# Kernel optimization log

Hardware: AMD Instinct MI355X
Metric: run time of the kernel (lower is better)

The kernel has to match this reference:

```python
import jax, jax.numpy as jnp
import numpy as np

N_NODES = 100000
N_EDGES = 1600000
IN_FEATS = 128
HID = 128      # 2 * n_hidden
OUT = 64       # n_hidden


def setup_inputs() -> dict:
    key = jax.random.key(0)
    ks = jax.random.split(key, 10)
    features = jax.random.normal(ks[0], (N_NODES, IN_FEATS), dtype=jnp.float32)
    src = jax.random.randint(ks[1], (N_EDGES,), 0, N_NODES)
    dst = jax.random.randint(ks[2], (N_EDGES,), 0, N_NODES)
    s0 = 1.0 / np.sqrt(IN_FEATS)
    s1 = 1.0 / np.sqrt(HID)
    W_self0 = jax.random.uniform(ks[3], (IN_FEATS, HID), minval=-s0, maxval=s0, dtype=jnp.float32)
    W_neigh0 = jax.random.uniform(ks[4], (IN_FEATS, HID), minval=-s0, maxval=s0, dtype=jnp.float32)
    b0 = jnp.zeros((HID,), dtype=jnp.float32)
    W_self1 = jax.random.uniform(ks[5], (HID, OUT), minval=-s1, maxval=s1, dtype=jnp.float32)
    W_neigh1 = jax.random.uniform(ks[6], (HID, OUT), minval=-s1, maxval=s1, dtype=jnp.float32)
    b1 = jnp.zeros((OUT,), dtype=jnp.float32)
    return {"features": features, "src": src, "dst": dst,
            "W_self0": W_self0, "W_neigh0": W_neigh0, "b0": b0,
            "W_self1": W_self1, "W_neigh1": W_neigh1, "b1": b1}


def _mean_agg(x, src, dst, n_nodes):
    # gather neighbor feats along edges, sum per destination, divide by in-degree
    summed = jax.ops.segment_sum(x[src], dst, num_segments=n_nodes)  # [N, d]
    deg = jax.ops.segment_sum(jnp.ones((src.shape[0],), x.dtype), dst, num_segments=n_nodes)
    deg = jnp.maximum(deg, 1.0)[:, None]
    return summed / deg


def _sage_layer(x, src, dst, W_self, W_neigh, b, act):
    agg = _mean_agg(x, src, dst, x.shape[0])
    out = x @ W_self + agg @ W_neigh + b
    return jax.nn.relu(out) if act else out


def reference(features, src, dst, W_self0, W_neigh0, b0, W_self1, W_neigh1, b1):
    h = _sage_layer(features, src, dst, W_self0, W_neigh0, b0, act=True)
    h = _sage_layer(h, src, dst, W_self1, W_neigh1, b1, act=False)
    return h
```

## Files before the change

kernel.cpp:

```cpp
#include <hip/hip_runtime.h>

#define N_NODES 100000
#define N_EDGES 1600000
#define CAP 56
#define OVF_CAP 8192
#define GBLK 782
#define BINS 391
#define BINCAP 4608
#define ABLK 1563

typedef unsigned int uint;
typedef unsigned short ushort;
typedef __attribute__((ext_vector_type(8))) short short8;
typedef __attribute__((ext_vector_type(4))) float f32x4;

__device__ __forceinline__ ushort f2bf(float f) {
  uint x = __float_as_uint(f);
  x += 0x7fffu + ((x >> 16) & 1u);
  return (ushort)(x >> 16);
}
__device__ __forceinline__ float bflo(uint u) {
  return __uint_as_float(u << 16);
}
__device__ __forceinline__ float bfhi(uint u) {
  return __uint_as_float(u & 0xffff0000u);
}
__device__ __forceinline__ f32x4 uplo(uint4 u) {
  return (f32x4){bflo(u.x), bfhi(u.x), bflo(u.y), bfhi(u.y)};
}
__device__ __forceinline__ f32x4 uphi(uint4 u) {
  return (f32x4){bflo(u.z), bfhi(u.z), bflo(u.w), bfhi(u.w)};
}

__global__ __launch_bounds__(256) void k_pb(
    const int* __restrict__ src, const int* __restrict__ dst,
    const float* __restrict__ feat, const float* __restrict__ Ws0,
    const float* __restrict__ Wn0, const float* __restrict__ Ws1,
    const float* __restrict__ Wn1, uint* __restrict__ gcursor,
    uint* __restrict__ binbuf, int* __restrict__ ovf_cnt,
    int* __restrict__ ovf, uint* __restrict__ fbfu, ushort* __restrict__ wp0,
    ushort* __restrict__ wp1) {
  __shared__ uint hist[BINS];
  __shared__ uint base[BINS];
  int b = blockIdx.x;
  int tid = threadIdx.x;
  if (b < GBLK) {
    for (int i = tid; i < BINS; i += 256) hist[i] = 0;
    __syncthreads();
    int e0 = b * 2048;
    uint val[8], bn[8], rk[8];
    int vld[8];
#pragma unroll
    for (int it = 0; it < 8; ++it) {
      int e = e0 + it * 256 + tid;
      vld[it] = (e < N_EDGES);
      if (vld[it]) {
        uint s = (uint)src[e];
        uint d = (uint)dst[e];
        bn[it] = d >> 8;
        rk[it] = atomicAdd(&hist[bn[it]], 1u);
        val[it] = s | ((d & 255u) << 17);
      }
    }
    __syncthreads();
    for (int i = tid; i < BINS; i += 256)
      base[i] = hist[i] ? atomicAdd(&gcursor[i], hist[i]) : 0u;
    __syncthreads();
#pragma unroll
    for (int it = 0; it < 8; ++it) {
      if (!vld[it]) continue;
      uint p = base[bn[it]] + rk[it];
      if (p < BINCAP) {
        binbuf[(size_t)bn[it] * BINCAP + p] = val[it];
      } else {
        int o = atomicAdd(ovf_cnt, 1);
        if (o < OVF_CAP) {
          ovf[2 * o] = (int)(val[it] & 0x1FFFFu);
          ovf[2 * o + 1] = (int)(bn[it] * 256 + (val[it] >> 17));
        }
      }
    }
    return;
  }
  if (b < GBLK + 25000) {
    int i = (b - GBLK) * 256 + tid;
    float2 v = reinterpret_cast<const float2*>(feat)[i];
    fbfu[i] = (uint)f2bf(v.x) | ((uint)f2bf(v.y) << 16);
    return;
  }
  int idx = (b - GBLK - 25000) * 256 + tid;
  if (idx < 32768) {
    int k = idx >> 7, n = idx & 127;
    float v = (k < 128) ? Ws0[k * 128 + n] : Wn0[(k - 128) * 128 + n];
    int s = k >> 5, q = (k >> 3) & 3, j = k & 7;
    int t = n >> 4, c = n & 15;
    wp0[(((s * 8 + t) * 64) + (q * 16 + c)) * 8 + j] = f2bf(v);
  } else {
    int i2 = idx - 32768;
    int k = i2 >> 7, n = i2 & 127;
    float v = (n < 64) ? Wn1[k * 64 + n] : Ws1[k * 64 + (n - 64)];
    int s = k >> 5, q = (k >> 3) & 3, j = k & 7;
    int t = n >> 4, c = n & 15;
    wp1[(((s * 8 + t) * 64) + (q * 16 + c)) * 8 + j] = f2bf(v);
  }
}

__global__ __launch_bounds__(256) void k_agg0(
    const uint4* __restrict__ fbf4, const uint* __restrict__ binbuf,
    const uint* __restrict__ gcursor, int* __restrict__ ovf_cnt,
    int* __restrict__ ovf, uint4* __restrict__ agg4) {
  __shared__ __attribute__((aligned(16))) int lbkt[64 * CAP];
  __shared__ uint lcnt[64];
  int bb = blockIdx.x;
  int tid = threadIdx.x;
  if (tid < 64) lcnt[tid] = 0;
  __syncthreads();
  int bin = bb >> 2, q2 = bb & 3;
  int ne = min((int)gcursor[bin], BINCAP);
  for (int i = tid; i < ne; i += 256) {
    uint v = binbuf[(size_t)bin * BINCAP + i];
    uint dl = v >> 17;
    if ((int)(dl >> 6) == q2) {
      int ldl = (int)(dl & 63u);
      uint pos = atomicAdd(&lcnt[ldl], 1u);
      if (pos < CAP) {
        lbkt[ldl * CAP + pos] = (int)(v & 0x1FFFFu);
      } else {
        int o = atomicAdd(ovf_cnt, 1);
        if (o < OVF_CAP) {
          ovf[2 * o] = (int)(v & 0x1FFFFu);
          ovf[2 * o + 1] = (bin * 256 + (int)dl) | (1 << 30);
        }
      }
    }
  }
  __syncthreads();
  int g = tid >> 4, li = tid & 15;
  const int4* lb4 = reinterpret_cast<const int4*>(lbkt);
  int oc = min(*ovf_cnt, OVF_CAP);
#pragma unroll
  for (int p = 0; p < 4; ++p) {
    int nl = p * 16 + g;
    int n = bb * 64 + nl;
    int c = (int)lcnt[nl];
    int kb = min(c, CAP);
    f32x4 accA = (f32x4){0.f, 0.f, 0.f, 0.f};
    f32x4 accB = (f32x4){0.f, 0.f, 0.f, 0.f};
    for (int j = 0; j < kb; j += 8) {
      int4 ia = lb4[nl * 14 + (j >> 2)];
      int4 ib = lb4[nl * 14 + (j >> 2) + 1];
      int s0 = ia.x;
      int s1 = (j + 1 < kb) ? ia.y : 0;
      int s2 = (j + 2 < kb) ? ia.z : 0;
      int s3 = (j + 3 < kb) ? ia.w : 0;
      int s4 = (j + 4 < kb) ? ib.x : 0;
      int s5 = (j + 5 < kb) ? ib.y : 0;
      int s6 = (j + 6 < kb) ? ib.z : 0;
      int s7 = (j + 7 < kb) ? ib.w : 0;
      uint4 u0 = fbf4[(size_t)s0 * 16 + li];
      uint4 u1 = fbf4[(size_t)s1 * 16 + li];
      uint4 u2 = fbf4[(size_t)s2 * 16 + li];
      uint4 u3 = fbf4[(size_t)s3 * 16 + li];
      uint4 u4 = fbf4[(size_t)s4 * 16 + li];
      uint4 u5 = fbf4[(size_t)s5 * 16 + li];
      uint4 u6 = fbf4[(size_t)s6 * 16 + li];
      uint4 u7 = fbf4[(size_t)s7 * 16 + li];
      float m1 = (j + 1 < kb) ? 1.f : 0.f;
      float m2 = (j + 2 < kb) ? 1.f : 0.f;
      float m3 = (j + 3 < kb) ? 1.f : 0.f;
      float m4 = (j + 4 < kb) ? 1.f : 0.f;
      float m5 = (j + 5 < kb) ? 1.f : 0.f;
      float m6 = (j + 6 < kb) ? 1.f : 0.f;
      float m7 = (j + 7 < kb) ? 1.f : 0.f;
      accA += uplo(u0);      accB += uphi(u0);
      accA += uplo(u1) * m1; accB += uphi(u1) * m1;
      accA += uplo(u2) * m2; accB += uphi(u2) * m2;
      accA += uplo(u3) * m3; accB += uphi(u3) * m3;
      accA += uplo(u4) * m4; accB += uphi(u4) * m4;
      accA += uplo(u5) * m5; accB += uphi(u5) * m5;
      accA += uplo(u6) * m6; accB += uphi(u6) * m6;
      accA += uplo(u7) * m7; accB += uphi(u7) * m7;
    }
    for (int i = 0; i < oc; ++i) {
      int df = ovf[2 * i + 1];
      if ((df & 0x1FFFF) == n) {
        uint4 u = fbf4[(size_t)ovf[2 * i] * 16 + li];
        accA += uplo(u);
        accB += uphi(u);
        c += ((df >> 30) & 1) ^ 1;
      }
    }
    float inv = 1.f / (float)max(c, 1);
    accA *= inv;
    accB *= inv;
    if (n < N_NODES) {
      uint4 o;
      o.x = (uint)f2bf(accA.x) | ((uint)f2bf(accA.y) << 16);
      o.y = (uint)f2bf(accA.z) | ((uint)f2bf(accA.w) << 16);
      o.z = (uint)f2bf(accB.x) | ((uint)f2bf(accB.y) << 16);
      o.w = (uint)f2bf(accB.z) | ((uint)f2bf(accB.w) << 16);
      agg4[(size_t)n * 16 + li] = o;
    }
  }
}

__global__ __launch_bounds__(256) void k_gemm0(
    const ushort* __restrict__ fbf, const ushort* aggb,
    const uint4* __restrict__ wp0g, const float* __restrict__ b0,
    ushort* h) {
  __shared__ uint4 wlds[4096];
  int tid = threadIdx.x;
#pragma unroll
  for (int i = 0; i < 16; ++i) wlds[i * 256 + tid] = wp0g[i * 256 + tid];
  __syncthreads();
  const short8* wl8 = reinterpret_cast<const short8*>(wlds);

  int lane = tid & 63, w = tid >> 6;
  int quad = lane >> 4, lm = lane & 15;
  int mw = blockIdx.x * 128 + (w >> 1) * 64;
  int tgb = (w & 1) * 4;

  f32x4 acc[4][4];
#pragma unroll
  for (int rt = 0; rt < 4; ++rt)
#pragma unroll
    for (int ct = 0; ct < 4; ++ct) acc[rt][ct] = (f32x4){0.f, 0.f, 0.f, 0.f};
  short8 az = {0, 0, 0, 0, 0, 0, 0, 0};

#pragma unroll
  for (int s = 0; s < 8; ++s) {
    const ushort* bsrc = (s < 4) ? fbf : aggb;
    int koff = (s & 3) * 32 + quad * 8;
    short8 a[4];
#pragma unroll
    for (int rt = 0; rt < 4; ++rt) {
      int row = mw + rt * 16 + lm;
      a[rt] = (row < N_NODES)
                  ? *reinterpret_cast<const short8*>(bsrc + (size_t)row * 128 + koff)
                  : az;
    }
#pragma unroll
    for (int ct = 0; ct < 4; ++ct) {
      short8 b = wl8[(s * 8 + tgb + ct) * 64 + lane];
#pragma unroll
      for (int rt = 0; rt < 4; ++rt)
        acc[rt][ct] =
            __builtin_amdgcn_mfma_f32_16x16x32_bf16(a[rt], b, acc[rt][ct], 0, 0, 0);
    }
  }

  __syncthreads();
  float bv[4];
#pragma unroll
  for (int ct = 0; ct < 4; ++ct) bv[ct] = b0[(tgb + ct) * 16 + lm];
#pragma unroll
  for (int rt = 0; rt < 4; ++rt)
#pragma unroll
    for (int ct = 0; ct < 4; ++ct)
#pragma unroll
      for (int i = 0; i < 4; ++i) {
        int row = mw + rt * 16 + quad * 4 + i;
        if (row < N_NODES) {
          int col = (tgb + ct) * 16 + lm;
          h[(size_t)row * 128 + col] = f2bf(fmaxf(acc[rt][ct][i] + bv[ct], 0.f));
        }
      }
}

__global__ __launch_bounds__(256) void k_gemm1(
    const ushort* __restrict__ h, const uint4* __restrict__ wp1g,
    const float* __restrict__ b1, ushort* __restrict__ hw,
    float* __restrict__ out) {
  __shared__ uint4 wlds[2048];
  int tid = threadIdx.x;
#pragma unroll
  for (int i = 0; i < 8; ++i) wlds[i * 256 + tid] = wp1g[i * 256 + tid];
  __syncthreads();
  const short8* wl8 = reinterpret_cast<const short8*>(wlds);

  int lane = tid & 63, w = tid >> 6;
  int quad = lane >> 4, lm = lane & 15;
  int mw = blockIdx.x * 128 + (w >> 1) * 64;
  int tgb = (w & 1) * 4;

  f32x4 acc[4][4];
#pragma unroll
  for (int rt = 0; rt < 4; ++rt)
#pragma unroll
    for (int ct = 0; ct < 4; ++ct) acc[rt][ct] = (f32x4){0.f, 0.f, 0.f, 0.f};
  short8 az = {0, 0, 0, 0, 0, 0, 0, 0};

#pragma unroll
  for (int s = 0; s < 4; ++s) {
    int koff = s * 32 + quad * 8;
    short8 a[4];
#pragma unroll
    for (int rt = 0; rt < 4; ++rt) {
      int row = mw + rt * 16 + lm;
      a[rt] = (row < N_NODES)
                  ? *reinterpret_cast<const short8*>(h + (size_t)row * 128 + koff)
                  : az;
    }
#pragma unroll
    for (int ct = 0; ct < 4; ++ct) {
      short8 b = wl8[(s * 8 + tgb + ct) * 64 + lane];
#pragma unroll
      for (int rt = 0; rt < 4; ++rt)
        acc[rt][ct] =
            __builtin_amdgcn_mfma_f32_16x16x32_bf16(a[rt], b, acc[rt][ct], 0, 0, 0);
    }
  }

  if ((w & 1) == 0) {
#pragma unroll
    for (int rt = 0; rt < 4; ++rt)
#pragma unroll
      for (int ct = 0; ct < 4; ++ct)
#pragma unroll
        for (int i = 0; i < 4; ++i) {
          int row = mw + rt * 16 + quad * 4 + i;
          if (row < N_NODES)
            hw[(size_t)row * 64 + ct * 16 + lm] = f2bf(acc[rt][ct][i]);
        }
  } else {
    float bv[4];
#pragma unroll
    for (int ct = 0; ct < 4; ++ct) bv[ct] = b1[ct * 16 + lm];
#pragma unroll
    for (int rt = 0; rt < 4; ++rt)
#pragma unroll
      for (int ct = 0; ct < 4; ++ct)
#pragma unroll
        for (int i = 0; i < 4; ++i) {
          int row = mw + rt * 16 + quad * 4 + i;
          if (row < N_NODES)
            out[(size_t)row * 64 + ct * 16 + lm] = acc[rt][ct][i] + bv[ct];
        }
  }
}

__global__ __launch_bounds__(256) void k_agg1(
    const uint4* __restrict__ hw4, const uint* __restrict__ binbuf,
    const uint* __restrict__ gcursor, int* __restrict__ ovf_cnt,
    int* __restrict__ ovf, float* __restrict__ out) {
  __shared__ __attribute__((aligned(16))) int lbkt[64 * CAP];
  __shared__ uint lcnt[64];
  int bb = blockIdx.x;
  int tid = threadIdx.x;
  if (tid < 64) lcnt[tid] = 0;
  __syncthreads();
  int bin = bb >> 2, q2 = bb & 3;
  int ne = min((int)gcursor[bin], BINCAP);
  for (int i = tid; i < ne; i += 256) {
    uint v = binbuf[(size_t)bin * BINCAP + i];
    uint dl = v >> 17;
    if ((int)(dl >> 6) == q2) {
      int ldl = (int)(dl & 63u);
      uint pos = atomicAdd(&lcnt[ldl], 1u);
      if (pos < CAP) lbkt[ldl * CAP + pos] = (int)(v & 0x1FFFFu);
    }
  }
  __syncthreads();
  int g = tid >> 3, li = tid & 7;
  const int4* lb4 = reinterpret_cast<const int4*>(lbkt);
  int oc = min(*ovf_cnt, OVF_CAP);
#pragma unroll
  for (int p = 0; p < 2; ++p) {
    int nl = p * 32 + g;
    int n = bb * 64 + nl;
    int c = (int)lcnt[nl];
    int kb = min(c, CAP);
    f32x4 accA = (f32x4){0.f, 0.f, 0.f, 0.f};
    f32x4 accB = (f32x4){0.f, 0.f, 0.f, 0.f};
    for (int j = 0; j < kb; j += 8) {
      int4 ia = lb4[nl * 14 + (j >> 2)];
      int4 ib = lb4[nl * 14 + (j >> 2) + 1];
      int s0 = ia.x;
      int s1 = (j + 1 < kb) ? ia.y : 0;
      int s2 = (j + 2 < kb) ? ia.z : 0;
      int s3 = (j + 3 < kb) ? ia.w : 0;
      int s4 = (j + 4 < kb) ? ib.x : 0;
      int s5 = (j + 5 < kb) ? ib.y : 0;
      int s6 = (j + 6 < kb) ? ib.z : 0;
      int s7 = (j + 7 < kb) ? ib.w : 0;
      uint4 u0 = hw4[(size_t)s0 * 8 + li];
      uint4 u1 = hw4[(size_t)s1 * 8 + li];
      uint4 u2 = hw4[(size_t)s2 * 8 + li];
      uint4 u3 = hw4[(size_t)s3 * 8 + li];
      uint4 u4 = hw4[(size_t)s4 * 8 + li];
      uint4 u5 = hw4[(size_t)s5 * 8 + li];
      uint4 u6 = hw4[(size_t)s6 * 8 + li];
      uint4 u7 = hw4[(size_t)s7 * 8 + li];
      float m1 = (j + 1 < kb) ? 1.f : 0.f;
      float m2 = (j + 2 < kb) ? 1.f : 0.f;
      float m3 = (j + 3 < kb) ? 1.f : 0.f;
      float m4 = (j + 4 < kb) ? 1.f : 0.f;
      float m5 = (j + 5 < kb) ? 1.f : 0.f;
      float m6 = (j + 6 < kb) ? 1.f : 0.f;
      float m7 = (j + 7 < kb) ? 1.f : 0.f;
      accA += uplo(u0);      accB += uphi(u0);
      accA += uplo(u1) * m1; accB += uphi(u1) * m1;
      accA += uplo(u2) * m2; accB += uphi(u2) * m2;
      accA += uplo(u3) * m3; accB += uphi(u3) * m3;
      accA += uplo(u4) * m4; accB += uphi(u4) * m4;
      accA += uplo(u5) * m5; accB += uphi(u5) * m5;
      accA += uplo(u6) * m6; accB += uphi(u6) * m6;
      accA += uplo(u7) * m7; accB += uphi(u7) * m7;
    }
    for (int i = 0; i < oc; ++i) {
      int df = ovf[2 * i + 1];
      if ((df & 0x1FFFF) == n) {
        uint4 u = hw4[(size_t)ovf[2 * i] * 8 + li];
        accA += uplo(u);
        accB += uphi(u);
        c += ((df >> 30) & 1) ^ 1;
      }
    }
    if (n < N_NODES) {
      float inv = 1.f / (float)max(c, 1);
      float* op = out + (size_t)n * 64 + li * 8;
      float4 c0 = *reinterpret_cast<float4*>(op);
      float4 c1 = *reinterpret_cast<float4*>(op + 4);
      c0.x += accA.x * inv;
      c0.y += accA.y * inv;
      c0.z += accA.z * inv;
      c0.w += accA.w * inv;
      c1.x += accB.x * inv;
      c1.y += accB.y * inv;
      c1.z += accB.z * inv;
      c1.w += accB.w * inv;
      *reinterpret_cast<float4*>(op) = c0;
      *reinterpret_cast<float4*>(op + 4) = c1;
    }
  }
}

extern "C" void kernel_launch(void* const* d_in, const int* in_sizes, int n_in,
                              void* d_out, int out_size, void* d_ws,
                              size_t ws_size, hipStream_t stream) {
  const float* feat = (const float*)d_in[0];
  const int* src = (const int*)d_in[1];
  const int* dst = (const int*)d_in[2];
  const float* Ws0 = (const float*)d_in[3];
  const float* Wn0 = (const float*)d_in[4];
  const float* b0 = (const float*)d_in[5];
  const float* Ws1 = (const float*)d_in[6];
  const float* Wn1 = (const float*)d_in[7];
  const float* b1 = (const float*)d_in[8];
  char* ws = (char*)d_ws;

  ushort* hbuf = (ushort*)(ws);
  int* ovf_cnt = (int*)(ws + 25600000);
  uint* gcursor = (uint*)(ws + 25600064);
  int* ovf = (int*)(ws + 25601664);
  uint* binbuf = (uint*)(ws + 26067200);
  ushort* fbf = (ushort*)(ws + 48467200);
  ushort* hw = (ushort*)(ws + 48467200);
  ushort* wp0 = (ushort*)(ws + 74067200);
  ushort* wp1 = (ushort*)(ws + 74132736);
  float* out = (float*)d_out;

  hipMemsetAsync(ws + 25600000, 0, 1664, stream);
  k_pb<<<GBLK + 25000 + 192, 256, 0, stream>>>(src, dst, feat, Ws0, Wn0, Ws1,
                                               Wn1, gcursor, binbuf, ovf_cnt,
                                               ovf, (uint*)fbf, wp0, wp1);
  k_agg0<<<ABLK, 256, 0, stream>>>((const uint4*)fbf, binbuf, gcursor, ovf_cnt,
                                   ovf, (uint4*)hbuf);
  k_gemm0<<<GBLK, 256, 0, stream>>>(fbf, hbuf, (const uint4*)wp0, b0, hbuf);
  k_gemm1<<<GBLK, 256, 0, stream>>>(hbuf, (const uint4*)wp1, b1, hw, out);
  k_agg1<<<ABLK, 256, 0, stream>>>((const uint4*)hw, binbuf, gcursor, ovf_cnt,
                                   ovf, out);
}
```

Baseline: 296.9 us.

## Bin edges per 64-node block, pad buckets with zero row, widen feature conversion

Edge binning now uses one bin per 64 destination nodes, so each aggregation block reads only its own edges and no longer scans and filters four times as many. Local buckets are pre-filled with the index of an all-zero sentinel row, written by the prep and gemm1 kernels, so the gather loop drops its per-element masks and runs 12 loads per step. The bf16 feature conversion handles four floats per thread with half as many blocks. Costs include a larger per-block histogram in shared memory, LDS prefill work, and reads of the zero row for padding slots.

```diff
diff --git a/kernel.cpp b/kernel.cpp
--- a/kernel.cpp
+++ b/kernel.cpp
@@ -2,12 +2,13 @@
 
 #define N_NODES 100000
 #define N_EDGES 1600000
-#define CAP 56
+#define CAP 60
 #define OVF_CAP 8192
 #define GBLK 782
-#define BINS 391
-#define BINCAP 4608
-#define ABLK 1563
+#define NBIN 1563
+#define BINCAP2 1280
+#define FBLK 12500
+#define ZROW 100000
 
 typedef unsigned int uint;
 typedef unsigned short ushort;
@@ -40,12 +41,12 @@
     uint* __restrict__ binbuf, int* __restrict__ ovf_cnt,
     int* __restrict__ ovf, uint* __restrict__ fbfu, ushort* __restrict__ wp0,
     ushort* __restrict__ wp1) {
-  __shared__ uint hist[BINS];
-  __shared__ uint base[BINS];
+  __shared__ uint hist[NBIN];
+  __shared__ uint base[NBIN];
   int b = blockIdx.x;
   int tid = threadIdx.x;
   if (b < GBLK) {
-    for (int i = tid; i < BINS; i += 256) hist[i] = 0;
+    for (int i = tid; i < NBIN; i += 256) hist[i] = 0;
     __syncthreads();
     int e0 = b * 2048;
     uint val[8], bn[8], rk[8];
@@ -57,38 +58,46 @@
       if (vld[it]) {
         uint s = (uint)src[e];
         uint d = (uint)dst[e];
-        bn[it] = d >> 8;
+        bn[it] = d >> 6;
         rk[it] = atomicAdd(&hist[bn[it]], 1u);
-        val[it] = s | ((d & 255u) << 17);
+        val[it] = s | ((d & 63u) << 17);
       }
     }
     __syncthreads();
-    for (int i = tid; i < BINS; i += 256)
+    for (int i = tid; i < NBIN; i += 256)
       base[i] = hist[i] ? atomicAdd(&gcursor[i], hist[i]) : 0u;
     __syncthreads();
 #pragma unroll
     for (int it = 0; it < 8; ++it) {
       if (!vld[it]) continue;
       uint p = base[bn[it]] + rk[it];
-      if (p < BINCAP) {
-        binbuf[(size_t)bn[it] * BINCAP + p] = val[it];
+      if (p < BINCAP2) {
+        binbuf[(size_t)bn[it] * BINCAP2 + p] = val[it];
       } else {
         int o = atomicAdd(ovf_cnt, 1);
         if (o < OVF_CAP) {
           ovf[2 * o] = (int)(val[it] & 0x1FFFFu);
-          ovf[2 * o + 1] = (int)(bn[it] * 256 + (val[it] >> 17));
+          ovf[2 * o + 1] = (int)(bn[it] * 64 + (val[it] >> 17));
         }
       }
     }
     return;
   }
-  if (b < GBLK + 25000) {
+  if (b < GBLK + FBLK) {
     int i = (b - GBLK) * 256 + tid;
-    float2 v = reinterpret_cast<const float2*>(feat)[i];
-    fbfu[i] = (uint)f2bf(v.x) | ((uint)f2bf(v.y) << 16);
+    float4 v = reinterpret_cast<const float4*>(feat)[i];
+    uint2 o;
+    o.x = (uint)f2bf(v.x) | ((uint)f2bf(v.y) << 16);
+    o.y = (uint)f2bf(v.z) | ((uint)f2bf(v.w) << 16);
+    reinterpret_cast<uint2*>(fbfu)[i] = o;
     return;
   }
-  int idx = (b - GBLK - 25000) * 256 + tid;
+  int wb = b - GBLK - FBLK;
+  if (wb >= 192) {
+    if (tid < 64) fbfu[ZROW * 64 + tid] = 0;
+    return;
+  }
+  int idx = wb * 256 + tid;
   if (idx < 32768) {
     int k = idx >> 7, n = idx & 127;
     float v = (k < 128) ? Ws0[k * 128 + n] : Wn0[(k - 128) * 128 + n];
@@ -114,23 +123,21 @@
   int bb = blockIdx.x;
   int tid = threadIdx.x;
   if (tid < 64) lcnt[tid] = 0;
-  __syncthreads();
-  int bin = bb >> 2, q2 = bb & 3;
-  int ne = min((int)gcursor[bin], BINCAP);
+#pragma unroll
+  for (int i = tid; i < 64 * CAP; i += 256) lbkt[i] = ZROW;
+  __syncthreads();
+  int ne = min((int)gcursor[bb], BINCAP2);
   for (int i = tid; i < ne; i += 256) {
-    uint v = binbuf[(size_t)bin * BINCAP + i];
-    uint dl = v >> 17;
-    if ((int)(dl >> 6) == q2) {
-      int ldl = (int)(dl & 63u);
-      uint pos = atomicAdd(&lcnt[ldl], 1u);
-      if (pos < CAP) {
-        lbkt[ldl * CAP + pos] = (int)(v & 0x1FFFFu);
-      } else {
-        int o = atomicAdd(ovf_cnt, 1);
-        if (o < OVF_CAP) {
-          ovf[2 * o] = (int)(v & 0x1FFFFu);
-          ovf[2 * o + 1] = (bin * 256 + (int)dl) | (1 << 30);
-        }
+    uint v = binbuf[(size_t)bb * BINCAP2 + i];
+    int ldl = (int)(v >> 17);
+    uint pos = atomicAdd(&lcnt[ldl], 1u);
+    if (pos < CAP) {
+      lbkt[ldl * CAP + pos] = (int)(v & 0x1FFFFu);
+    } else {
+      int o = atomicAdd(ovf_cnt, 1);
+      if (o < OVF_CAP) {
+        ovf[2 * o] = (int)(v & 0x1FFFFu);
+        ovf[2 * o + 1] = (bb * 64 + ldl) | (1 << 30);
       }
     }
   }
@@ -146,40 +153,34 @@
     int kb = min(c, CAP);
     f32x4 accA = (f32x4){0.f, 0.f, 0.f, 0.f};
     f32x4 accB = (f32x4){0.f, 0.f, 0.f, 0.f};
-    for (int j = 0; j < kb; j += 8) {
-      int4 ia = lb4[nl * 14 + (j >> 2)];
-      int4 ib = lb4[nl * 14 + (j >> 2) + 1];
-      int s0 = ia.x;
-      int s1 = (j + 1 < kb) ? ia.y : 0;
-      int s2 = (j + 2 < kb) ? ia.z : 0;
-      int s3 = (j + 3 < kb) ? ia.w : 0;
-      int s4 = (j + 4 < kb) ? ib.x : 0;
-      int s5 = (j + 5 < kb) ? ib.y : 0;
-      int s6 = (j + 6 < kb) ? ib.z : 0;
-      int s7 = (j + 7 < kb) ? ib.w : 0;
-      uint4 u0 = fbf4[(size_t)s0 * 16 + li];
-      uint4 u1 = fbf4[(size_t)s1 * 16 + li];
-      uint4 u2 = fbf4[(size_t)s2 * 16 + li];
-      uint4 u3 = fbf4[(size_t)s3 * 16 + li];
-      uint4 u4 = fbf4[(size_t)s4 * 16 + li];
-      uint4 u5 = fbf4[(size_t)s5 * 16 + li];
-      uint4 u6 = fbf4[(size_t)s6 * 16 + li];
-      uint4 u7 = fbf4[(size_t)s7 * 16 + li];
-      float m1 = (j + 1 < kb) ? 1.f : 0.f;
-      float m2 = (j + 2 < kb) ? 1.f : 0.f;
-      float m3 = (j + 3 < kb) ? 1.f : 0.f;
-      float m4 = (j + 4 < kb) ? 1.f : 0.f;
-      float m5 = (j + 5 < kb) ? 1.f : 0.f;
-      float m6 = (j + 6 < kb) ? 1.f : 0.f;
-      float m7 = (j + 7 < kb) ? 1.f : 0.f;
-      accA += uplo(u0);      accB += uphi(u0);
-      accA += uplo(u1) * m1; accB += uphi(u1) * m1;
-      accA += uplo(u2) * m2; accB += uphi(u2) * m2;
-      accA += uplo(u3) * m3; accB += uphi(u3) * m3;
-      accA += uplo(u4) * m4; accB += uphi(u4) * m4;
-      accA += uplo(u5) * m5; accB += uphi(u5) * m5;
-      accA += uplo(u6) * m6; accB += uphi(u6) * m6;
-      accA += uplo(u7) * m7; accB += uphi(u7) * m7;
+    for (int j = 0; j < kb; j += 12) {
+      int4 ia = lb4[nl * 15 + (j >> 2)];
+      int4 ib = lb4[nl * 15 + (j >> 2) + 1];
+      int4 ic = lb4[nl * 15 + (j >> 2) + 2];
+      uint4 u0 = fbf4[(size_t)ia.x * 16 + li];
+      uint4 u1 = fbf4[(size_t)ia.y * 16 + li];
+      uint4 u2 = fbf4[(size_t)ia.z * 16 + li];
+      uint4 u3 = fbf4[(size_t)ia.w * 16 + li];
+      uint4 u4 = fbf4[(size_t)ib.x * 16 + li];
+      uint4 u5 = fbf4[(size_t)ib.y * 16 + li];
+      uint4 u6 = fbf4[(size_t)ib.z * 16 + li];
+      uint4 u7 = fbf4[(size_t)ib.w * 16 + li];
+      uint4 u8 = fbf4[(size_t)ic.x * 16 + li];
+      uint4 u9 = fbf4[(size_t)ic.y * 16 + li];
+      uint4 ua = fbf4[(size_t)ic.z * 16 + li];
+      uint4 ub = fbf4[(size_t)ic.w * 16 + li];
+      accA += uplo(u0); accB += uphi(u0);
+      accA += uplo(u1); accB += uphi(u1);
+      accA += uplo(u2); accB += uphi(u2);
+      accA += uplo(u3); accB += uphi(u3);
+      accA += uplo(u4); accB += uphi(u4);
+      accA += uplo(u5); accB += uphi(u5);
+      accA += uplo(u6); accB += uphi(u6);
+      accA += uplo(u7); accB += uphi(u7);
+      accA += uplo(u8); accB += uphi(u8);
+      accA += uplo(u9); accB += uphi(u9);
+      accA += uplo(ua); accB += uphi(ua);
+      accA += uplo(ub); accB += uphi(ub);
     }
     for (int i = 0; i < oc; ++i) {
       int df = ovf[2 * i + 1];
@@ -273,6 +274,8 @@
     float* __restrict__ out) {
   __shared__ uint4 wlds[2048];
   int tid = threadIdx.x;
+  if (blockIdx.x == 0 && tid < 8)
+    reinterpret_cast<uint4*>(hw)[ZROW * 8 + tid] = make_uint4(0, 0, 0, 0);
 #pragma unroll
   for (int i = 0; i < 8; ++i) wlds[i * 256 + tid] = wp1g[i * 256 + tid];
   __syncthreads();
@@ -348,17 +351,15 @@
   int bb = blockIdx.x;
   int tid = threadIdx.x;
   if (tid < 64) lcnt[tid] = 0;
-  __syncthreads();
-  int bin = bb >> 2, q2 = bb & 3;
-  int ne = min((int)gcursor[bin], BINCAP);
+#pragma unroll
+  for (int i = tid; i < 64 * CAP; i += 256) lbkt[i] = ZROW;
+  __syncthreads();
+  int ne = min((int)gcursor[bb], BINCAP2);
   for (int i = tid; i < ne; i += 256) {
-    uint v = binbuf[(size_t)bin * BINCAP + i];
-    uint dl = v >> 17;
-    if ((int)(dl >> 6) == q2) {
-      int ldl = (int)(dl & 63u);
-      uint pos = atomicAdd(&lcnt[ldl], 1u);
-      if (pos < CAP) lbkt[ldl * CAP + pos] = (int)(v & 0x1FFFFu);
-    }
+    uint v = binbuf[(size_t)bb * BINCAP2 + i];
+    int ldl = (int)(v >> 17);
+    uint pos = atomicAdd(&lcnt[ldl], 1u);
+    if (pos < CAP) lbkt[ldl * CAP + pos] = (int)(v & 0x1FFFFu);
   }
   __syncthreads();
   int g = tid >> 3, li = tid & 7;
@@ -372,40 +373,34 @@
     int kb = min(c, CAP);
     f32x4 accA = (f32x4){0.f, 0.f, 0.f, 0.f};
     f32x4 accB = (f32x4){0.f, 0.f, 0.f, 0.f};
-    for (int j = 0; j < kb; j += 8) {
-      int4 ia = lb4[nl * 14 + (j >> 2)];
-      int4 ib = lb4[nl * 14 + (j >> 2) + 1];
-      int s0 = ia.x;
-      int s1 = (j + 1 < kb) ? ia.y : 0;
-      int s2 = (j + 2 < kb) ? ia.z : 0;
-      int s3 = (j + 3 < kb) ? ia.w : 0;
-      int s4 = (j + 4 < kb) ? ib.x : 0;
-      int s5 = (j + 5 < kb) ? ib.y : 0;
-      int s6 = (j + 6 < kb) ? ib.z : 0;
-      int s7 = (j + 7 < kb) ? ib.w : 0;
-      uint4 u0 = hw4[(size_t)s0 * 8 + li];
-      uint4 u1 = hw4[(size_t)s1 * 8 + li];
-      uint4 u2 = hw4[(size_t)s2 * 8 + li];
-      uint4 u3 = hw4[(size_t)s3 * 8 + li];
-      uint4 u4 = hw4[(size_t)s4 * 8 + li];
-      uint4 u5 = hw4[(size_t)s5 * 8 + li];
-      uint4 u6 = hw4[(size_t)s6 * 8 + li];
-      uint4 u7 = hw4[(size_t)s7 * 8 + li];
-      float m1 = (j + 1 < kb) ? 1.f : 0.f;
-      float m2 = (j + 2 < kb) ? 1.f : 0.f;
-      float m3 = (j + 3 < kb) ? 1.f : 0.f;
-      float m4 = (j + 4 < kb) ? 1.f : 0.f;
-      float m5 = (j + 5 < kb) ? 1.f : 0.f;
-      float m6 = (j + 6 < kb) ? 1.f : 0.f;
-      float m7 = (j + 7 < kb) ? 1.f : 0.f;
-      accA += uplo(u0);      accB += uphi(u0);
-      accA += uplo(u1) * m1; accB += uphi(u1) * m1;
-      accA += uplo(u2) * m2; accB += uphi(u2) * m2;
-      accA += uplo(u3) * m3; accB += uphi(u3) * m3;
-      accA += uplo(u4) * m4; accB += uphi(u4) * m4;
-      accA += uplo(u5) * m5; accB += uphi(u5) * m5;
-      accA += uplo(u6) * m6; accB += uphi(u6) * m6;
-      accA += uplo(u7) * m7; accB += uphi(u7) * m7;
+    for (int j = 0; j < kb; j += 12) {
+      int4 ia = lb4[nl * 15 + (j >> 2)];
+      int4 ib = lb4[nl * 15 + (j >> 2) + 1];
+      int4 ic = lb4[nl * 15 + (j >> 2) + 2];
+      uint4 u0 = hw4[(size_t)ia.x * 8 + li];
+      uint4 u1 = hw4[(size_t)ia.y * 8 + li];
+      uint4 u2 = hw4[(size_t)ia.z * 8 + li];
+      uint4 u3 = hw4[(size_t)ia.w * 8 + li];
+      uint4 u4 = hw4[(size_t)ib.x * 8 + li];
+      uint4 u5 = hw4[(size_t)ib.y * 8 + li];
+      uint4 u6 = hw4[(size_t)ib.z * 8 + li];
+      uint4 u7 = hw4[(size_t)ib.w * 8 + li];
+      uint4 u8 = hw4[(size_t)ic.x * 8 + li];
+      uint4 u9 = hw4[(size_t)ic.y * 8 + li];
+      uint4 ua = hw4[(size_t)ic.z * 8 + li];
+      uint4 ub = hw4[(size_t)ic.w * 8 + li];
+      accA += uplo(u0); accB += uphi(u0);
+      accA += uplo(u1); accB += uphi(u1);
+      accA += uplo(u2); accB += uphi(u2);
+      accA += uplo(u3); accB += uphi(u3);
+      accA += uplo(u4); accB += uphi(u4);
+      accA += uplo(u5); accB += uphi(u5);
+      accA += uplo(u6); accB += uphi(u6);
+      accA += uplo(u7); accB += uphi(u7);
+      accA += uplo(u8); accB += uphi(u8);
+      accA += uplo(u9); accB += uphi(u9);
+      accA += uplo(ua); accB += uphi(ua);
+      accA += uplo(ub); accB += uphi(ub);
     }
     for (int i = 0; i < oc; ++i) {
       int df = ovf[2 * i + 1];
@@ -452,22 +447,22 @@
   ushort* hbuf = (ushort*)(ws);
   int* ovf_cnt = (int*)(ws + 25600000);
   uint* gcursor = (uint*)(ws + 25600064);
-  int* ovf = (int*)(ws + 25601664);
-  uint* binbuf = (uint*)(ws + 26067200);
-  ushort* fbf = (ushort*)(ws + 48467200);
-  ushort* hw = (ushort*)(ws + 48467200);
-  ushort* wp0 = (ushort*)(ws + 74067200);
-  ushort* wp1 = (ushort*)(ws + 74132736);
+  int* ovf = (int*)(ws + 25606400);
+  uint* binbuf = (uint*)(ws + 25671936);
+  ushort* fbf = (ushort*)(ws + 33674496);
+  ushort* hw = (ushort*)(ws + 33674496);
+  ushort* wp0 = (ushort*)(ws + 59274752);
+  ushort* wp1 = (ushort*)(ws + 59340288);
   float* out = (float*)d_out;
 
-  hipMemsetAsync(ws + 25600000, 0, 1664, stream);
-  k_pb<<<GBLK + 25000 + 192, 256, 0, stream>>>(src, dst, feat, Ws0, Wn0, Ws1,
-                                               Wn1, gcursor, binbuf, ovf_cnt,
-                                               ovf, (uint*)fbf, wp0, wp1);
-  k_agg0<<<ABLK, 256, 0, stream>>>((const uint4*)fbf, binbuf, gcursor, ovf_cnt,
+  hipMemsetAsync(ws + 25600000, 0, 6400, stream);
+  k_pb<<<GBLK + FBLK + 193, 256, 0, stream>>>(src, dst, feat, Ws0, Wn0, Ws1,
+                                              Wn1, gcursor, binbuf, ovf_cnt,
+                                              ovf, (uint*)fbf, wp0, wp1);
+  k_agg0<<<NBIN, 256, 0, stream>>>((const uint4*)fbf, binbuf, gcursor, ovf_cnt,
                                    ovf, (uint4*)hbuf);
   k_gemm0<<<GBLK, 256, 0, stream>>>(fbf, hbuf, (const uint4*)wp0, b0, hbuf);
   k_gemm1<<<GBLK, 256, 0, stream>>>(hbuf, (const uint4*)wp1, b1, hw, out);
-  k_agg1<<<ABLK, 256, 0, stream>>>((const uint4*)hw, binbuf, gcursor, ovf_cnt,
+  k_agg1<<<NBIN, 256, 0, stream>>>((const uint4*)hw, binbuf, gcursor, ovf_cnt,
                                    ovf, out);
 }
```

Result: faster. 288.1 us (-3.0%).
